# Performance work log

Hardware: AMD Instinct MI355X
Metric: run time of the kernel (lower is better)

Reference implementation:

```python
import jax, jax.numpy as jnp
import numpy as np
from jax import lax

B, T, N, E, H = 8, 12, 716, 10, 64
DIN = 1 + H  # GCN input dim = x(1) concat state(H)
CS = 1       # conv_steps (predict_time)


def setup_inputs() -> dict:
    key = jax.random.key(0)
    ks = jax.random.split(key, 26)
    def rn(i, shape, s=0.1):
        return jax.random.normal(ks[i], shape, jnp.float32) * s
    data = jax.random.normal(ks[0], (B, T, N, 1), jnp.float32)
    tid = jax.random.uniform(ks[1], (B, T, N, 1), jnp.float32)          # time-of-day in [0,1)
    diw = jax.random.randint(ks[2], (B, T, N, 1), 0, 7).astype(jnp.float32)  # day-of-week
    source = jnp.concatenate([data, tid, diw], axis=-1)
    return dict(
        source=source,
        node_embeddings=rn(3, (N, E), 1.0),
        tid_emb=rn(4, (288, E), 1.0),
        diw_emb=rn(5, (7, E), 1.0),
        wp_g=rn(6, (2, E, 2, DIN, 2 * H)),
        bp_g=rn(7, (2, E, 2 * H)),
        fc1W_g=rn(8, (2, 16, DIN)), fc1b_g=rn(9, (2, 16)),
        fc2W_g=rn(10, (2, 2, 16)), fc2b_g=rn(11, (2, 2)),
        fc3W_g=rn(12, (2, E, 2)), fc3b_g=rn(13, (2, E)),
        wp_u=rn(14, (2, E, 2, DIN, H)),
        bp_u=rn(15, (2, E, H)),
        fc1W_u=rn(16, (2, 16, DIN)), fc1b_u=rn(17, (2, 16)),
        fc2W_u=rn(18, (2, 2, 16)), fc2b_u=rn(19, (2, 2)),
        fc3W_u=rn(20, (2, E, 2)), fc3b_u=rn(21, (2, E)),
        predW=rn(22, (2, T, CS, H)),
        predB=rn(23, (2, T)),
        skipW=rn(24, (T, CS, H)),
        skipB=rn(25, (T,)),
    )


def _gcn(x, emb_t, static, wp, bp, fc):
    # x: [B,N,DIN], emb_t: [B,N,E], static: [N,E]
    fc1W, fc1b, fc2W, fc2b, fc3W, fc3b = fc
    h = jax.nn.sigmoid(x @ fc1W.T + fc1b)
    h = jax.nn.sigmoid(h @ fc2W.T + fc2b)
    x_ = h @ fc3W.T + fc3b                            # [B,N,E]
    nodevec = jnp.tanh(emb_t * x_)                    # [B,N,E]
    graph = jax.nn.relu(jnp.einsum('bne,bme->bnm', nodevec, nodevec))
    d = jnp.sum(graph, axis=-1) ** -0.5               # [B,N]
    L = d[:, :, None] * graph * d[:, None, :]         # D^-1/2 A D^-1/2 support
    xg2 = jnp.einsum('bnm,bmc->bnc', L, x)
    w = jnp.einsum('ne,ekio->nkio', static, wp)       # [N,2,DIN,out]
    b = static @ bp                                   # [N,out]
    # support1 is identity -> x_g1 == x
    return (jnp.einsum('bni,nio->bno', x, w[:, 0])
            + jnp.einsum('bni,nio->bno', xg2, w[:, 1]) + b)


def _gru_layer(x_seq, emb_seq, static, gate_p, upd_p):
    # x_seq: [T,B,N,1], emb_seq: [T,B,N,E]
    wp_g, bp_g, fc_g = gate_p
    wp_u, bp_u, fc_u = upd_p
    Hd = wp_u.shape[-1]
    def step(state, inp):
        x, emb = inp
        xs = jnp.concatenate([x, state], axis=-1)
        zr = jax.nn.sigmoid(_gcn(xs, emb, static, wp_g, bp_g, fc_g))
        z, r = jnp.split(zr, 2, axis=-1)
        cand = jnp.concatenate([x, z * state], axis=-1)
        hc = jnp.tanh(_gcn(cand, emb, static, wp_u, bp_u, fc_u))
        h = r * state + (1 - r) * hc
        return h, h
    h0 = jnp.zeros(x_seq.shape[1:3] + (Hd,), x_seq.dtype)
    _, hs = lax.scan(step, h0, (x_seq, emb_seq))
    return hs  # [T,B,N,H]


def reference(source, node_embeddings, tid_emb, diw_emb,
              wp_g, bp_g, fc1W_g, fc1b_g, fc2W_g, fc2b_g, fc3W_g, fc3b_g,
              wp_u, bp_u, fc1W_u, fc1b_u, fc2W_u, fc2b_u, fc3W_u, fc3b_u,
              predW, predB, skipW, skipB):
    x = source[..., :1]                                   # [B,T,N,1]
    tid_idx = (source[..., 1] * 288).astype(jnp.int32)
    diw_idx = source[..., 2].astype(jnp.int32)
    emb = node_embeddings * tid_emb[tid_idx] * diw_emb[diw_idx]  # [B,T,N,E]
    x_t = jnp.moveaxis(x, 1, 0)                           # [T,B,N,1]
    emb_t = jnp.moveaxis(emb, 1, 0)                       # [T,B,N,E]
    cur = x_t
    predict = jnp.zeros((x.shape[0], T, x.shape[2], 1), x.dtype)
    for c in range(2):  # two structurally distinct GRU layers
        gate_p = (wp_g[c], bp_g[c], (fc1W_g[c], fc1b_g[c], fc2W_g[c], fc2b_g[c], fc3W_g[c], fc3b_g[c]))
        upd_p = (wp_u[c], bp_u[c], (fc1W_u[c], fc1b_u[c], fc2W_u[c], fc2b_u[c], fc3W_u[c], fc3b_u[c]))
        hs = _gru_layer(cur, emb_t, node_embeddings, gate_p, upd_p)
        ci = jnp.moveaxis(hs[-CS:], 0, 1)                 # [B,CS,N,H] (dropout is identity in eval)
        out = jnp.einsum('bcnh,och->bon', ci, predW[c]) + predB[c][None, :, None]
        predict = predict + out[..., None]                # [B,T,N,1]
        if c == 0:
            sk = jnp.einsum('bcnh,och->bon', ci, skipW) + skipB[None, :, None]
            cur = x_t - jnp.moveaxis(sk[..., None], 1, 0)
    return predict
```

## Files before the change

### kernel.cpp

```cpp
#include <hip/hip_runtime.h>
#include <math.h>

#define BB 8
#define TT 12
#define NN 716
#define EE 10
#define HH 64
#define DIN 65
#define OG 128
#define OU 64
#define XSP 68
#define JS 32
#define JRX 23
#define NTN 128
#define NP 768
#define NI4 17
#define NVP 12

__device__ __forceinline__ float sigmf(float x){ return 1.0f/(1.0f+__expf(-x)); }

__global__ void k_emb(const float* __restrict__ src, const float* __restrict__ ne,
                      const float* __restrict__ te, const float* __restrict__ de,
                      float* __restrict__ emb, float* __restrict__ cur){
  int idx = blockIdx.x*256 + threadIdx.x;
  if (idx >= BB*TT*NN) return;
  int n = idx % NN; int t = (idx/NN) % TT; int b = idx/(NN*TT);
  const float* s = src + (size_t)idx*3;
  float x = s[0];
  int ti = (int)(s[1]*288.0f);
  int di = (int)(s[2]);
  size_t eo = ((size_t)b*TT + t)*NN*EE + (size_t)n*EE;
  #pragma unroll
  for (int e=0;e<EE;e++)
    emb[eo+e] = ne[n*EE+e]*te[ti*EE+e]*de[di*EE+e];
  cur[((size_t)t*BB + b)*NN + n] = x;
}

__global__ __launch_bounds__(256) void k_prep_w4m(
    const float* __restrict__ ne, const float* __restrict__ wp_g,
    const float* __restrict__ wp_u, float* __restrict__ wg4,
    float* __restrict__ wu4)
{
  __shared__ float wps[EE*4*OG];
  int which = blockIdx.z;
  const float* wp = which ? wp_u : wp_g;
  float* w4 = which ? wu4 : wg4;
  int O = which ? OU : OG;
  int ki4 = blockIdx.x;
  int nq  = blockIdx.y;
  int k = ki4/NI4, i4 = ki4 - k*NI4;
  int tid = threadIdx.x;
  for (int idx=tid; idx<EE*4*O; idx+=256){
    int e = idx/(4*O); int rem = idx - e*4*O; int sub = rem/O; int o = rem - sub*O;
    int i = i4*4 + sub;
    wps[idx] = (i<DIN) ? wp[(((size_t)e*2+k)*DIN+i)*O + o] : 0.f;
  }
  __syncthreads();
  int NG = 256/O;
  int o = tid & (O-1), ng = tid / O;
  int n1 = nq*179, n2 = min(NN, n1+179);
  for (int n = n1+ng; n < n2; n += NG){
    float4 a = {0.f,0.f,0.f,0.f};
    #pragma unroll
    for (int e=0;e<EE;e++){
      float nef = ne[n*EE+e];
      a.x += nef*wps[e*4*O + 0*O + o];
      a.y += nef*wps[e*4*O + 1*O + o];
      a.z += nef*wps[e*4*O + 2*O + o];
      a.w += nef*wps[e*4*O + 3*O + o];
    }
    ((float4*)w4)[((size_t)(n*2+k)*NI4 + i4)*O + o] = a;
  }
}

__global__ void k_misc(const float* __restrict__ ne,
                       const float* __restrict__ bp_g, const float* __restrict__ bp_u,
                       float* __restrict__ bg, float* __restrict__ bu,
                       float* __restrict__ h, const float* __restrict__ cur_c,
                       const float* __restrict__ f1W, const float* __restrict__ f1b,
                       const float* __restrict__ f2W, const float* __restrict__ f2b,
                       const float* __restrict__ f3W, const float* __restrict__ f3b,
                       const float* __restrict__ emb,
                       float* __restrict__ xsg, float* __restrict__ nv){
  int mt = blockIdx.x*256 + threadIdx.x;
  int MT = gridDim.x*256;
  for (int i=mt; i<BB*NN*HH; i+=MT) h[i] = 0.f;
  for (int i=mt; i<NN*OG; i+=MT){
    int o=i&(OG-1), n=i>>7; float a=0.f;
    #pragma unroll
    for (int e=0;e<EE;e++) a += ne[n*EE+e]*bp_g[e*OG+o];
    bg[i]=a;
  }
  for (int i=mt; i<NN*OU; i+=MT){
    int o=i&(OU-1), n=i>>6; float a=0.f;
    #pragma unroll
    for (int e=0;e<EE;e++) a += ne[n*EE+e]*bp_u[e*OU+o];
    bu[i]=a;
  }
  for (int idx=mt; idx<BB*NN; idx+=MT){
    int b=idx/NN, n=idx-b*NN;
    float x = cur_c[(size_t)b*NN + n];
    float* xr = xsg + (size_t)idx*XSP;
    xr[0]=x;
    #pragma unroll
    for (int i2=1;i2<XSP;i2++) xr[i2]=0.f;
    float h1[16];
    #pragma unroll
    for (int k=0;k<16;k++) h1[k]=sigmf(f1b[k]+f1W[k*DIN]*x);
    float h2[2];
    #pragma unroll
    for (int k=0;k<2;k++){
      float s=f2b[k];
      #pragma unroll
      for (int q=0;q<16;q++) s+=f2W[k*16+q]*h1[q];
      h2[k]=sigmf(s);
    }
    #pragma unroll
    for (int e=0;e<EE;e++){
      float xe=f3b[e]+f3W[e*2]*h2[0]+f3W[e*2+1]*h2[1];
      nv[(size_t)idx*EE+e]=tanhf(emb[(((size_t)b*TT+0)*NN+n)*EE+e]*xe);
    }
  }
}

__global__ __launch_bounds__(256) void k_xg2d(
    const float* __restrict__ nv, const float* __restrict__ xs,
    float* __restrict__ parts, float* __restrict__ dout)
{
  __shared__ __align__(16) float nvs[NN*NVP];
  __shared__ __align__(16) float xss[32][XSP];
  __shared__ __align__(16) float gs[32][NTN+4];
  __shared__ float dls[32];
  int js = blockIdx.x, b = blockIdx.y;
  int tid = threadIdx.x;
  int j0 = js*JRX;
  int cnt = NN - j0; if (cnt > JRX) cnt = JRX;
  {
    const float* nvb = nv + (size_t)b*NN*EE;
    for (int idx=tid; idx<NN*EE; idx+=256){
      int n = idx/10, e = idx - n*10;
      nvs[n*NVP+e] = nvb[idx];
    }
  }
  __syncthreads();
  int jg = tid>>5, ns = tid&31;
  float bv[4][EE];
  #pragma unroll
  for (int r=0;r<4;r++){
    int jr = jg*4+r;
    if (jr < cnt){
      const float* bp2 = &nvs[(j0+jr)*NVP];
      float4 b0 = *(const float4*)bp2;
      float4 b1 = *(const float4*)(bp2+4);
      float2 b2 = *(const float2*)(bp2+8);
      bv[r][0]=b0.x; bv[r][1]=b0.y; bv[r][2]=b0.z; bv[r][3]=b0.w;
      bv[r][4]=b1.x; bv[r][5]=b1.y; bv[r][6]=b1.z; bv[r][7]=b1.w;
      bv[r][8]=b2.x; bv[r][9]=b2.y;
    } else {
      #pragma unroll
      for (int e=0;e<EE;e++) bv[r][e]=0.f;
    }
  }
  {
    float sums[4]={0.f,0.f,0.f,0.f};
    for (int n=ns; n<NN; n+=32){
      const float* ap = &nvs[n*NVP];
      float4 a0 = *(const float4*)ap;
      float4 a1 = *(const float4*)(ap+4);
      float2 a2 = *(const float2*)(ap+8);
      float av[10] = {a0.x,a0.y,a0.z,a0.w,a1.x,a1.y,a1.z,a1.w,a2.x,a2.y};
      #pragma unroll
      for (int r=0;r<4;r++){
        float s=0.f;
        #pragma unroll
        for (int e=0;e<EE;e++) s += bv[r][e]*av[e];
        sums[r] += fmaxf(s,0.f);
      }
    }
    #pragma unroll
    for (int r=0;r<4;r++){
      float s = sums[r];
      s += __shfl_xor(s,1,64); s += __shfl_xor(s,2,64);
      s += __shfl_xor(s,4,64); s += __shfl_xor(s,8,64);
      s += __shfl_xor(s,16,64);
      sums[r] = s;
    }
    if (ns==0){
      #pragma unroll
      for (int r=0;r<4;r++){
        int jr = jg*4+r;
        if (jr < cnt){
          float dv = rsqrtf(sums[r]);
          dls[jr] = dv;
          dout[b*NN + j0 + jr] = dv;
        }
      }
    }
  }
  __syncthreads();
  for (int idx=tid; idx<32*XSP; idx+=256){
    int r = idx/XSP, ii = idx - r*XSP;
    float v = 0.f;
    if (r < cnt && ii <= 64)
      v = dls[r]*xs[((size_t)b*NN+j0+r)*XSP + ii];
    xss[r][ii] = v;
  }
  int ng = tid >> 3, ig = tid & 7;
  int ng4 = tid & 31;
  for (int nc=0; nc<6; ++nc){
    int n0 = nc*NTN;
    {
      float g[4][4];
      #pragma unroll
      for (int r=0;r<4;r++){ g[r][0]=0;g[r][1]=0;g[r][2]=0;g[r][3]=0; }
      #pragma unroll
      for (int s2=0;s2<4;s2++){
        int n = n0 + ng4*4 + s2;
        if (n < NN){
          const float* ap = &nvs[n*NVP];
          float4 a0 = *(const float4*)ap;
          float4 a1 = *(const float4*)(ap+4);
          float2 a2 = *(const float2*)(ap+8);
          float av[10] = {a0.x,a0.y,a0.z,a0.w,a1.x,a1.y,a1.z,a1.w,a2.x,a2.y};
          #pragma unroll
          for (int r=0;r<4;r++){
            float s=0.f;
            #pragma unroll
            for (int e=0;e<EE;e++) s += bv[r][e]*av[e];
            g[r][s2] = s;
          }
        }
      }
      #pragma unroll
      for (int r=0;r<4;r++){
        float4 v = { fmaxf(g[r][0],0.f), fmaxf(g[r][1],0.f),
                     fmaxf(g[r][2],0.f), fmaxf(g[r][3],0.f) };
        *(float4*)&gs[jg*4+r][ng4*4] = v;
      }
    }
    __syncthreads();
    {
      float acc[4][8];
      #pragma unroll
      for (int r=0;r<4;r++)
        #pragma unroll
        for (int s2=0;s2<8;s2++) acc[r][s2]=0.f;
      for (int jj=0; jj<cnt; ++jj){
        float4 g4  = *(const float4*)&gs[jj][ng*4];
        float4 x4a = *(const float4*)&xss[jj][ig*8];
        float4 x4b = *(const float4*)&xss[jj][ig*8+4];
        float gr[4] = {g4.x, g4.y, g4.z, g4.w};
        float xr[8] = {x4a.x,x4a.y,x4a.z,x4a.w, x4b.x,x4b.y,x4b.z,x4b.w};
        #pragma unroll
        for (int r=0;r<4;r++)
          #pragma unroll
          for (int s2=0;s2<8;s2++) acc[r][s2] += gr[r]*xr[s2];
      }
      #pragma unroll
      for (int r=0;r<4;r++){
        int n = n0 + ng*4 + r;
        float4 v0 = { acc[r][0], acc[r][1], acc[r][2], acc[r][3] };
        float4 v1 = { acc[r][4], acc[r][5], acc[r][6], acc[r][7] };
        size_t base = (((size_t)js*BB+b)*NP+n)*XSP;
        *(float4*)&parts[base + ig*8]     = v0;
        *(float4*)&parts[base + ig*8 + 4] = v1;
      }
      if (tid < NTN){
        float s = 0.f;
        for (int jj=0; jj<cnt; ++jj) s += gs[jj][tid]*xss[jj][64];
        parts[(((size_t)js*BB+b)*NP + n0+tid)*XSP + 64] = s;
      }
    }
    __syncthreads();
  }
}

__global__ __launch_bounds__(256, 4) void k_tr_gate(
    const float* __restrict__ wg, const float* __restrict__ bg,
    const float* __restrict__ parts, const float* __restrict__ d,
    const float* __restrict__ xsg,
    const float* __restrict__ cur_ct, const float* __restrict__ h,
    const float* __restrict__ emb, int t,
    const float* __restrict__ f1W, const float* __restrict__ f1b,
    const float* __restrict__ f2W, const float* __restrict__ f2b,
    const float* __restrict__ f3W, const float* __restrict__ f3b,
    float* __restrict__ rbuf, float* __restrict__ xsu, float* __restrict__ nv)
{
  __shared__ float xg2s[BB][XSP];
  __shared__ float xss[BB][XSP];
  __shared__ float cs[BB][DIN];
  __shared__ float h1s[BB][16];
  __shared__ float h2s[BB][2];
  int n = blockIdx.x;
  int tid = threadIdx.x;
  for (int idx=tid; idx<BB*XSP; idx+=256){
    int b = idx/XSP, i = idx - b*XSP;
    float s = 0.f;
    if (i < 65){
      #pragma unroll 8
      for (int js2=0; js2<JS; js2++)
        s += parts[(((size_t)js2*BB+b)*NP+n)*XSP + i];
      s *= d[b*NN+n];
    }
    xg2s[b][i] = s;
  }
  for (int idx=tid; idx<BB*XSP; idx+=256){
    int b = idx/XSP, i = idx - b*XSP;
    xss[b][i] = (i<65) ? xsg[((size_t)b*NN+n)*XSP + i] : 0.f;
  }
  __syncthreads();
  {
    int o = tid & 127, half = tid >> 7;
    const float4* w0p = (const float4*)wg + ((size_t)n*2+0)*NI4*OG + o;
    const float4* w1p = w0p + (size_t)NI4*OG;
    float bgv = bg[n*OG+o];
    float acc[4]; acc[0]=bgv; acc[1]=bgv; acc[2]=bgv; acc[3]=bgv;
    #pragma unroll 2
    for (int i4=0;i4<NI4;i4++){
      float4 w0 = w0p[(size_t)i4*OG];
      float4 w1 = w1p[(size_t)i4*OG];
      int i = i4*4;
      #pragma unroll
      for (int bb=0;bb<4;bb++){
        int b = 2*bb+half;
        acc[bb] += xss[b][i]*w0.x + xss[b][i+1]*w0.y
                 + xss[b][i+2]*w0.z + xss[b][i+3]*w0.w
                 + xg2s[b][i]*w1.x + xg2s[b][i+1]*w1.y
                 + xg2s[b][i+2]*w1.z + xg2s[b][i+3]*w1.w;
      }
    }
    #pragma unroll
    for (int bb=0;bb<4;bb++){
      int b = 2*bb+half;
      float v = sigmf(acc[bb]);
      if (o < 64){
        float cv = v * h[((size_t)b*NN+n)*HH + o];
        xsu[((size_t)b*NN+n)*XSP + 1 + o] = cv;
        cs[b][1+o] = cv;
      } else {
        rbuf[((size_t)b*NN+n)*HH + (o-64)] = v;
      }
    }
    if (o == 64){
      #pragma unroll
      for (int bb=0;bb<4;bb++){
        int b = 2*bb+half;
        float x = cur_ct[(size_t)b*NN+n];
        cs[b][0] = x;
        xsu[((size_t)b*NN+n)*XSP] = x;
      }
    }
  }
  __syncthreads();
  if (tid < BB*16){
    int b=tid>>4, k=tid&15;
    const float* wr = f1W + k*DIN;
    float s = f1b[k];
    #pragma unroll
    for (int i=0;i<DIN;i++) s += cs[b][i]*wr[i];
    h1s[b][k] = sigmf(s);
  }
  __syncthreads();
  if (tid < BB*2){
    int b=tid>>1, k=tid&1;
    float s = f2b[k];
    #pragma unroll
    for (int q2=0;q2<16;q2++) s += h1s[b][q2]*f2W[k*16+q2];
    h2s[b][k] = sigmf(s);
  }
  __syncthreads();
  if (tid < BB*EE){
    int b=tid/EE, e=tid-b*EE;
    float xe = f3b[e] + f3W[e*2]*h2s[b][0] + f3W[e*2+1]*h2s[b][1];
    nv[((size_t)b*NN+n)*EE+e] = tanhf(emb[(((size_t)b*TT+t)*NN+n)*EE+e]*xe);
  }
}

__global__ __launch_bounds__(256, 4) void k_tr_upd(
    const float* __restrict__ wu, const float* __restrict__ bu,
    const float* __restrict__ parts, const float* __restrict__ d,
    const float* __restrict__ xsu,
    const float* __restrict__ rbuf, float* __restrict__ h,
    float* __restrict__ cur, int c, int t,
    const float* __restrict__ emb,
    const float* __restrict__ f1W, const float* __restrict__ f1b,
    const float* __restrict__ f2W, const float* __restrict__ f2b,
    const float* __restrict__ f3W, const float* __restrict__ f3b,
    float* __restrict__ xsg, float* __restrict__ nv,
    const float* __restrict__ predW, const float* __restrict__ predB,
    const float* __restrict__ skipW, const float* __restrict__ skipB,
    float* __restrict__ out)
{
  __shared__ float xg2s[BB][XSP];
  __shared__ float xss[BB][XSP];
  __shared__ float hs[BB][HH];
  __shared__ float h1s[BB][16];
  __shared__ float h2s[BB][2];
  __shared__ float xns[BB];
  int n = blockIdx.x;
  int tid = threadIdx.x;
  for (int idx=tid; idx<BB*XSP; idx+=256){
    int b = idx/XSP, i = idx - b*XSP;
    float s = 0.f;
    if (i < 65){
      #pragma unroll 8
      for (int js2=0; js2<JS; js2++)
        s += parts[(((size_t)js2*BB+b)*NP+n)*XSP + i];
      s *= d[b*NN+n];
    }
    xg2s[b][i] = s;
  }
  for (int idx=tid; idx<BB*XSP; idx+=256){
    int b = idx/XSP, i = idx - b*XSP;
    xss[b][i] = (i<65) ? xsu[((size_t)b*NN+n)*XSP + i] : 0.f;
  }
  __syncthreads();
  {
    int o = tid & 63, grp = tid >> 6;
    const float4* w0p = (const float4*)wu + ((size_t)n*2+0)*NI4*OU + o;
    const float4* w1p = w0p + (size_t)NI4*OU;
    float acc[2];
    acc[0] = bu[n*OU+o]; acc[1] = acc[0];
    #pragma unroll 2
    for (int i4=0;i4<NI4;i4++){
      float4 w0 = w0p[(size_t)i4*OU];
      float4 w1 = w1p[(size_t)i4*OU];
      int i = i4*4;
      #pragma unroll
      for (int bb=0;bb<2;bb++){
        int b = grp + 4*bb;
        acc[bb] += xss[b][i]*w0.x + xss[b][i+1]*w0.y
                 + xss[b][i+2]*w0.z + xss[b][i+3]*w0.w
                 + xg2s[b][i]*w1.x + xg2s[b][i+1]*w1.y
                 + xg2s[b][i+2]*w1.z + xg2s[b][i+3]*w1.w;
      }
    }
    #pragma unroll
    for (int bb=0;bb<2;bb++){
      int b = grp + 4*bb;
      float hc = tanhf(acc[bb]);
      float r = rbuf[((size_t)b*NN+n)*HH+o];
      float hold = h[((size_t)b*NN+n)*HH+o];
      float hn = r*hold + (1.f-r)*hc;
      h[((size_t)b*NN+n)*HH+o] = hn;
      hs[b][o] = hn;
    }
  }
  __syncthreads();
  if (t < TT-1){
    if (tid < BB){
      float x = cur[(((size_t)c*TT + (t+1))*BB + tid)*NN + n];
      xns[tid] = x;
      xsg[((size_t)tid*NN+n)*XSP] = x;
    }
    for (int idx=tid; idx<BB*HH; idx+=256){
      int b = idx>>6, oo = idx&63;
      xsg[((size_t)b*NN+n)*XSP + 1 + oo] = hs[b][oo];
    }
    __syncthreads();
    if (tid < BB*16){
      int b=tid>>4, k=tid&15;
      const float* wr = f1W + k*DIN;
      float s = f1b[k] + wr[0]*xns[b];
      #pragma unroll
      for (int oo=0;oo<HH;oo++) s += hs[b][oo]*wr[1+oo];
      h1s[b][k] = sigmf(s);
    }
    __syncthreads();
    if (tid < BB*2){
      int b=tid>>1, k=tid&1;
      float s = f2b[k];
      #pragma unroll
      for (int q2=0;q2<16;q2++) s += h1s[b][q2]*f2W[k*16+q2];
      h2s[b][k] = sigmf(s);
    }
    __syncthreads();
    if (tid < BB*EE){
      int b=tid/EE, e=tid-b*EE;
      float xe = f3b[e] + f3W[e*2]*h2s[b][0] + f3W[e*2+1]*h2s[b][1];
      nv[((size_t)b*NN+n)*EE+e] =
        tanhf(emb[(((size_t)b*TT+(t+1))*NN+n)*EE+e]*xe);
    }
  } else {
    if (tid < BB*TT){
      int b = tid/TT, ot = tid - b*TT;
      const float* pw = predW + ((size_t)c*TT + ot)*HH;
      float pv = predB[c*TT+ot];
      #pragma unroll
      for (int q2=0;q2<HH;q2++) pv += hs[b][q2]*pw[q2];
      size_t oi = ((size_t)b*TT+ot)*NN + n;
      if (c == 0){
        out[oi] = pv;
        const float* sw = skipW + (size_t)ot*HH;
        float sk = skipB[ot];
        #pragma unroll
        for (int q2=0;q2<HH;q2++) sk += hs[b][q2]*sw[q2];
        cur[(((size_t)TT+ot)*BB + b)*NN + n] =
            cur[((size_t)ot*BB + b)*NN + n] - sk;
      } else {
        out[oi] += pv;
      }
    }
  }
}

extern "C" void kernel_launch(void* const* d_in, const int* in_sizes, int n_in,
                              void* d_out, int out_size, void* d_ws, size_t ws_size,
                              hipStream_t stream){
  const float* src  = (const float*)d_in[0];
  const float* ne   = (const float*)d_in[1];
  const float* te   = (const float*)d_in[2];
  const float* de   = (const float*)d_in[3];
  const float* wp_g = (const float*)d_in[4];
  const float* bp_g = (const float*)d_in[5];
  const float* f1W_g= (const float*)d_in[6];
  const float* f1b_g= (const float*)d_in[7];
  const float* f2W_g= (const float*)d_in[8];
  const float* f2b_g= (const float*)d_in[9];
  const float* f3W_g= (const float*)d_in[10];
  const float* f3b_g= (const float*)d_in[11];
  const float* wp_u = (const float*)d_in[12];
  const float* bp_u = (const float*)d_in[13];
  const float* f1W_u= (const float*)d_in[14];
  const float* f1b_u= (const float*)d_in[15];
  const float* f2W_u= (const float*)d_in[16];
  const float* f2b_u= (const float*)d_in[17];
  const float* f3W_u= (const float*)d_in[18];
  const float* f3b_u= (const float*)d_in[19];
  const float* predW= (const float*)d_in[20];
  const float* predB= (const float*)d_in[21];
  const float* skipW= (const float*)d_in[22];
  const float* skipB= (const float*)d_in[23];

  float* ws   = (float*)d_ws;
  float* emb  = ws;
  float* cur  = emb  + (size_t)BB*TT*NN*EE;
  float* wg   = cur  + (size_t)2*TT*BB*NN;
  float* bg   = wg   + (size_t)NN*2*NI4*OG*4;
  float* wu   = bg   + (size_t)NN*OG;
  float* bu   = wu   + (size_t)NN*2*NI4*OU*4;
  float* h    = bu   + (size_t)NN*OU;
  float* xsg  = h    + (size_t)BB*NN*HH;
  float* xsu  = xsg  + (size_t)BB*NN*XSP;
  float* nv   = xsu  + (size_t)BB*NN*XSP;
  float* dbuf = nv   + (size_t)BB*NN*EE;
  float* parts= dbuf + (size_t)BB*NN;
  float* rbuf = parts+ (size_t)JS*BB*NP*XSP;
  float* outp = (float*)d_out;

  k_emb<<<(BB*TT*NN+255)/256, 256, 0, stream>>>(src, ne, te, de, emb, cur);

  for (int c=0;c<2;c++){
    k_prep_w4m<<<dim3(2*NI4,4,2),256,0,stream>>>(ne,
        wp_g + (size_t)c*EE*2*DIN*OG, wp_u + (size_t)c*EE*2*DIN*OU, wg, wu);
    k_misc<<<1024,256,0,stream>>>(ne, bp_g + (size_t)c*EE*OG, bp_u + (size_t)c*EE*OU,
        bg, bu, h, cur + (size_t)c*TT*BB*NN,
        f1W_g + c*16*DIN, f1b_g + c*16, f2W_g + c*32, f2b_g + c*2,
        f3W_g + c*EE*2, f3b_g + c*EE, emb, xsg, nv);
    for (int t=0;t<TT;t++){
      k_xg2d<<<dim3(JS,BB),256,0,stream>>>(nv, xsg, parts, dbuf);
      k_tr_gate<<<NN,256,0,stream>>>(wg, bg, parts, dbuf, xsg,
          cur + ((size_t)c*TT+t)*BB*NN, h, emb, t,
          f1W_u + c*16*DIN, f1b_u + c*16, f2W_u + c*32, f2b_u + c*2,
          f3W_u + c*EE*2, f3b_u + c*EE, rbuf, xsu, nv);
      k_xg2d<<<dim3(JS,BB),256,0,stream>>>(nv, xsu, parts, dbuf);
      k_tr_upd<<<NN,256,0,stream>>>(wu, bu, parts, dbuf, xsu, rbuf, h,
          cur, c, t, emb,
          f1W_g + c*16*DIN, f1b_g + c*16, f2W_g + c*32, f2b_g + c*2,
          f3W_g + c*EE*2, f3b_g + c*EE,
          xsg, nv, predW, predB, skipW, skipB, outp);
    }
  }
}
```

Baseline: 2.968 ms.

## Double k_xg2d threads to 512 and merge prep kernels into one launch

The graph/aggregation kernel now runs with 512 threads per block. Each thread computes one graph row against 8 nodes, accumulates a 4x4 output tile instead of 4x8, and the degree reduction is done across full 64-lane wavefronts. The intent is more parallelism and latency hiding in the per-timestep kernel, which is launched 48 times and only has 256 blocks. Separately, the weight-prep and misc init kernels are fused into one launch using a third grid-z slice, which saves one launch per layer. The cost is fewer FMAs per shared-memory load and more block-level synchronisation pressure.

Result: slower. 3.030 ms (+2.1%).

```diff
diff --git a/kernel.cpp b/kernel.cpp
--- a/kernel.cpp
+++ b/kernel.cpp
@@ -36,94 +36,94 @@
   cur[((size_t)t*BB + b)*NN + n] = x;
 }
 
-__global__ __launch_bounds__(256) void k_prep_w4m(
+__global__ __launch_bounds__(256) void k_prep_all(
     const float* __restrict__ ne, const float* __restrict__ wp_g,
     const float* __restrict__ wp_u, float* __restrict__ wg4,
-    float* __restrict__ wu4)
+    float* __restrict__ wu4,
+    const float* __restrict__ bp_g, const float* __restrict__ bp_u,
+    float* __restrict__ bg, float* __restrict__ bu,
+    float* __restrict__ h, const float* __restrict__ cur_c,
+    const float* __restrict__ f1W, const float* __restrict__ f1b,
+    const float* __restrict__ f2W, const float* __restrict__ f2b,
+    const float* __restrict__ f3W, const float* __restrict__ f3b,
+    const float* __restrict__ emb,
+    float* __restrict__ xsg, float* __restrict__ nv)
 {
   __shared__ float wps[EE*4*OG];
-  int which = blockIdx.z;
-  const float* wp = which ? wp_u : wp_g;
-  float* w4 = which ? wu4 : wg4;
-  int O = which ? OU : OG;
-  int ki4 = blockIdx.x;
-  int nq  = blockIdx.y;
-  int k = ki4/NI4, i4 = ki4 - k*NI4;
+  int z = blockIdx.z;
   int tid = threadIdx.x;
-  for (int idx=tid; idx<EE*4*O; idx+=256){
-    int e = idx/(4*O); int rem = idx - e*4*O; int sub = rem/O; int o = rem - sub*O;
-    int i = i4*4 + sub;
-    wps[idx] = (i<DIN) ? wp[(((size_t)e*2+k)*DIN+i)*O + o] : 0.f;
-  }
-  __syncthreads();
-  int NG = 256/O;
-  int o = tid & (O-1), ng = tid / O;
-  int n1 = nq*179, n2 = min(NN, n1+179);
-  for (int n = n1+ng; n < n2; n += NG){
-    float4 a = {0.f,0.f,0.f,0.f};
-    #pragma unroll
-    for (int e=0;e<EE;e++){
-      float nef = ne[n*EE+e];
-      a.x += nef*wps[e*4*O + 0*O + o];
-      a.y += nef*wps[e*4*O + 1*O + o];
-      a.z += nef*wps[e*4*O + 2*O + o];
-      a.w += nef*wps[e*4*O + 3*O + o];
-    }
-    ((float4*)w4)[((size_t)(n*2+k)*NI4 + i4)*O + o] = a;
+  if (z < 2){
+    const float* wp = z ? wp_u : wp_g;
+    float* w4 = z ? wu4 : wg4;
+    int O = z ? OU : OG;
+    int ki4 = blockIdx.x;
+    int nq  = blockIdx.y;
+    int k = ki4/NI4, i4 = ki4 - k*NI4;
+    for (int idx=tid; idx<EE*4*O; idx+=256){
+      int e = idx/(4*O); int rem = idx - e*4*O; int sub = rem/O; int o = rem - sub*O;
+      int i = i4*4 + sub;
+      wps[idx] = (i<DIN) ? wp[(((size_t)e*2+k)*DIN+i)*O + o] : 0.f;
+    }
+    __syncthreads();
+    int NG = 256/O;
+    int o = tid & (O-1), ng = tid / O;
+    int n1 = nq*179, n2 = min(NN, n1+179);
+    for (int n = n1+ng; n < n2; n += NG){
+      float4 a = {0.f,0.f,0.f,0.f};
+      #pragma unroll
+      for (int e=0;e<EE;e++){
+        float nef = ne[n*EE+e];
+        a.x += nef*wps[e*4*O + 0*O + o];
+        a.y += nef*wps[e*4*O + 1*O + o];
+        a.z += nef*wps[e*4*O + 2*O + o];
+        a.w += nef*wps[e*4*O + 3*O + o];
+      }
+      ((float4*)w4)[((size_t)(n*2+k)*NI4 + i4)*O + o] = a;
+    }
+  } else {
+    int mt = (blockIdx.x*4 + blockIdx.y)*256 + tid;
+    const int MT = 136*256;
+    for (int i=mt; i<BB*NN*HH; i+=MT) h[i] = 0.f;
+    for (int i=mt; i<NN*OG; i+=MT){
+      int o=i&(OG-1), n=i>>7; float a=0.f;
+      #pragma unroll
+      for (int e=0;e<EE;e++) a += ne[n*EE+e]*bp_g[e*OG+o];
+      bg[i]=a;
+    }
+    for (int i=mt; i<NN*OU; i+=MT){
+      int o=i&(OU-1), n=i>>6; float a=0.f;
+      #pragma unroll
+      for (int e=0;e<EE;e++) a += ne[n*EE+e]*bp_u[e*OU+o];
+      bu[i]=a;
+    }
+    for (int idx=mt; idx<BB*NN; idx+=MT){
+      int b=idx/NN, n=idx-b*NN;
+      float x = cur_c[(size_t)b*NN + n];
+      float* xr = xsg + (size_t)idx*XSP;
+      xr[0]=x;
+      #pragma unroll
+      for (int i2=1;i2<XSP;i2++) xr[i2]=0.f;
+      float h1[16];
+      #pragma unroll
+      for (int k=0;k<16;k++) h1[k]=sigmf(f1b[k]+f1W[k*DIN]*x);
+      float h2[2];
+      #pragma unroll
+      for (int k=0;k<2;k++){
+        float s=f2b[k];
+        #pragma unroll
+        for (int q=0;q<16;q++) s+=f2W[k*16+q]*h1[q];
+        h2[k]=sigmf(s);
+      }
+      #pragma unroll
+      for (int e=0;e<EE;e++){
+        float xe=f3b[e]+f3W[e*2]*h2[0]+f3W[e*2+1]*h2[1];
+        nv[(size_t)idx*EE+e]=tanhf(emb[(((size_t)b*TT+0)*NN+n)*EE+e]*xe);
+      }
+    }
   }
 }
 
-__global__ void k_misc(const float* __restrict__ ne,
-                       const float* __restrict__ bp_g, const float* __restrict__ bp_u,
-                       float* __restrict__ bg, float* __restrict__ bu,
-                       float* __restrict__ h, const float* __restrict__ cur_c,
-                       const float* __restrict__ f1W, const float* __restrict__ f1b,
-                       const float* __restrict__ f2W, const float* __restrict__ f2b,
-                       const float* __restrict__ f3W, const float* __restrict__ f3b,
-                       const float* __restrict__ emb,
-                       float* __restrict__ xsg, float* __restrict__ nv){
-  int mt = blockIdx.x*256 + threadIdx.x;
-  int MT = gridDim.x*256;
-  for (int i=mt; i<BB*NN*HH; i+=MT) h[i] = 0.f;
-  for (int i=mt; i<NN*OG; i+=MT){
-    int o=i&(OG-1), n=i>>7; float a=0.f;
-    #pragma unroll
-    for (int e=0;e<EE;e++) a += ne[n*EE+e]*bp_g[e*OG+o];
-    bg[i]=a;
-  }
-  for (int i=mt; i<NN*OU; i+=MT){
-    int o=i&(OU-1), n=i>>6; float a=0.f;
-    #pragma unroll
-    for (int e=0;e<EE;e++) a += ne[n*EE+e]*bp_u[e*OU+o];
-    bu[i]=a;
-  }
-  for (int idx=mt; idx<BB*NN; idx+=MT){
-    int b=idx/NN, n=idx-b*NN;
-    float x = cur_c[(size_t)b*NN + n];
-    float* xr = xsg + (size_t)idx*XSP;
-    xr[0]=x;
-    #pragma unroll
-    for (int i2=1;i2<XSP;i2++) xr[i2]=0.f;
-    float h1[16];
-    #pragma unroll
-    for (int k=0;k<16;k++) h1[k]=sigmf(f1b[k]+f1W[k*DIN]*x);
-    float h2[2];
-    #pragma unroll
-    for (int k=0;k<2;k++){
-      float s=f2b[k];
-      #pragma unroll
-      for (int q=0;q<16;q++) s+=f2W[k*16+q]*h1[q];
-      h2[k]=sigmf(s);
-    }
-    #pragma unroll
-    for (int e=0;e<EE;e++){
-      float xe=f3b[e]+f3W[e*2]*h2[0]+f3W[e*2+1]*h2[1];
-      nv[(size_t)idx*EE+e]=tanhf(emb[(((size_t)b*TT+0)*NN+n)*EE+e]*xe);
-    }
-  }
-}
-
-__global__ __launch_bounds__(256) void k_xg2d(
+__global__ __launch_bounds__(512) void k_xg2d(
     const float* __restrict__ nv, const float* __restrict__ xs,
     float* __restrict__ parts, float* __restrict__ dout)
 {
@@ -137,58 +137,58 @@
   int cnt = NN - j0; if (cnt > JRX) cnt = JRX;
   {
     const float* nvb = nv + (size_t)b*NN*EE;
-    for (int idx=tid; idx<NN*EE; idx+=256){
+    for (int idx=tid; idx<NN*EE; idx+=512){
       int n = idx/10, e = idx - n*10;
       nvs[n*NVP+e] = nvb[idx];
     }
   }
   __syncthreads();
-  int jg = tid>>5, ns = tid&31;
-  float bv[4][EE];
-  #pragma unroll
-  for (int r=0;r<4;r++){
-    int jr = jg*4+r;
-    if (jr < cnt){
-      const float* bp2 = &nvs[(j0+jr)*NVP];
-      float4 b0 = *(const float4*)bp2;
-      float4 b1 = *(const float4*)(bp2+4);
-      float2 b2 = *(const float2*)(bp2+8);
-      bv[r][0]=b0.x; bv[r][1]=b0.y; bv[r][2]=b0.z; bv[r][3]=b0.w;
-      bv[r][4]=b1.x; bv[r][5]=b1.y; bv[r][6]=b1.z; bv[r][7]=b1.w;
-      bv[r][8]=b2.x; bv[r][9]=b2.y;
-    } else {
-      #pragma unroll
-      for (int e=0;e<EE;e++) bv[r][e]=0.f;
-    }
-  }
   {
-    float sums[4]={0.f,0.f,0.f,0.f};
-    for (int n=ns; n<NN; n+=32){
+    int wv = tid>>6, lane = tid&63;
+    float bvd[3][EE];
+    #pragma unroll
+    for (int r=0;r<3;r++){
+      int jr = wv*3+r;
+      if (jr < cnt){
+        const float* bp2 = &nvs[(j0+jr)*NVP];
+        float4 b0 = *(const float4*)bp2;
+        float4 b1 = *(const float4*)(bp2+4);
+        float2 b2 = *(const float2*)(bp2+8);
+        bvd[r][0]=b0.x; bvd[r][1]=b0.y; bvd[r][2]=b0.z; bvd[r][3]=b0.w;
+        bvd[r][4]=b1.x; bvd[r][5]=b1.y; bvd[r][6]=b1.z; bvd[r][7]=b1.w;
+        bvd[r][8]=b2.x; bvd[r][9]=b2.y;
+      } else {
+        #pragma unroll
+        for (int e=0;e<EE;e++) bvd[r][e]=0.f;
+      }
+    }
+    float sums[3]={0.f,0.f,0.f};
+    for (int n=lane; n<NN; n+=64){
       const float* ap = &nvs[n*NVP];
       float4 a0 = *(const float4*)ap;
       float4 a1 = *(const float4*)(ap+4);
       float2 a2 = *(const float2*)(ap+8);
       float av[10] = {a0.x,a0.y,a0.z,a0.w,a1.x,a1.y,a1.z,a1.w,a2.x,a2.y};
       #pragma unroll
-      for (int r=0;r<4;r++){
+      for (int r=0;r<3;r++){
         float s=0.f;
         #pragma unroll
-        for (int e=0;e<EE;e++) s += bv[r][e]*av[e];
+        for (int e=0;e<EE;e++) s += bvd[r][e]*av[e];
         sums[r] += fmaxf(s,0.f);
       }
     }
     #pragma unroll
-    for (int r=0;r<4;r++){
+    for (int r=0;r<3;r++){
       float s = sums[r];
       s += __shfl_xor(s,1,64); s += __shfl_xor(s,2,64);
       s += __shfl_xor(s,4,64); s += __shfl_xor(s,8,64);
-      s += __shfl_xor(s,16,64);
+      s += __shfl_xor(s,16,64); s += __shfl_xor(s,32,64);
       sums[r] = s;
     }
-    if (ns==0){
-      #pragma unroll
-      for (int r=0;r<4;r++){
-        int jr = jg*4+r;
+    if (lane==0){
+      #pragma unroll
+      for (int r=0;r<3;r++){
+        int jr = wv*3+r;
         if (jr < cnt){
           float dv = rsqrtf(sums[r]);
           dls[jr] = dv;
@@ -198,72 +198,73 @@
     }
   }
   __syncthreads();
-  for (int idx=tid; idx<32*XSP; idx+=256){
+  for (int idx=tid; idx<32*XSP; idx+=512){
     int r = idx/XSP, ii = idx - r*XSP;
     float v = 0.f;
     if (r < cnt && ii <= 64)
       v = dls[r]*xs[((size_t)b*NN+j0+r)*XSP + ii];
     xss[r][ii] = v;
   }
-  int ng = tid >> 3, ig = tid & 7;
-  int ng4 = tid & 31;
+  int jrow = tid >> 4;
+  int ng3  = tid & 15;
+  float bvg[EE];
+  if (jrow < cnt){
+    const float* bp2 = &nvs[(j0+jrow)*NVP];
+    float4 b0 = *(const float4*)bp2;
+    float4 b1 = *(const float4*)(bp2+4);
+    float2 b2 = *(const float2*)(bp2+8);
+    bvg[0]=b0.x; bvg[1]=b0.y; bvg[2]=b0.z; bvg[3]=b0.w;
+    bvg[4]=b1.x; bvg[5]=b1.y; bvg[6]=b1.z; bvg[7]=b1.w;
+    bvg[8]=b2.x; bvg[9]=b2.y;
+  } else {
+    #pragma unroll
+    for (int e=0;e<EE;e++) bvg[e]=0.f;
+  }
+  int ngg = tid >> 4;
+  int ig  = tid & 15;
   for (int nc=0; nc<6; ++nc){
     int n0 = nc*NTN;
     {
-      float g[4][4];
-      #pragma unroll
-      for (int r=0;r<4;r++){ g[r][0]=0;g[r][1]=0;g[r][2]=0;g[r][3]=0; }
-      #pragma unroll
-      for (int s2=0;s2<4;s2++){
-        int n = n0 + ng4*4 + s2;
+      float g[8];
+      #pragma unroll
+      for (int s2=0;s2<8;s2++){
+        int n = n0 + ng3*8 + s2;
+        float s = 0.f;
         if (n < NN){
           const float* ap = &nvs[n*NVP];
           float4 a0 = *(const float4*)ap;
           float4 a1 = *(const float4*)(ap+4);
           float2 a2 = *(const float2*)(ap+8);
-          float av[10] = {a0.x,a0.y,a0.z,a0.w,a1.x,a1.y,a1.z,a1.w,a2.x,a2.y};
-          #pragma unroll
-          for (int r=0;r<4;r++){
-            float s=0.f;
-            #pragma unroll
-            for (int e=0;e<EE;e++) s += bv[r][e]*av[e];
-            g[r][s2] = s;
-          }
+          s = bvg[0]*a0.x + bvg[1]*a0.y + bvg[2]*a0.z + bvg[3]*a0.w
+            + bvg[4]*a1.x + bvg[5]*a1.y + bvg[6]*a1.z + bvg[7]*a1.w
+            + bvg[8]*a2.x + bvg[9]*a2.y;
         }
-      }
-      #pragma unroll
-      for (int r=0;r<4;r++){
-        float4 v = { fmaxf(g[r][0],0.f), fmaxf(g[r][1],0.f),
-                     fmaxf(g[r][2],0.f), fmaxf(g[r][3],0.f) };
-        *(float4*)&gs[jg*4+r][ng4*4] = v;
-      }
+        g[s2] = fmaxf(s, 0.f);
+      }
+      float4 v0 = { g[0],g[1],g[2],g[3] };
+      float4 v1 = { g[4],g[5],g[6],g[7] };
+      *(float4*)&gs[jrow][ng3*8]   = v0;
+      *(float4*)&gs[jrow][ng3*8+4] = v1;
     }
     __syncthreads();
     {
-      float acc[4][8];
-      #pragma unroll
-      for (int r=0;r<4;r++)
-        #pragma unroll
-        for (int s2=0;s2<8;s2++) acc[r][s2]=0.f;
+      float acc[4][4];
+      #pragma unroll
+      for (int r=0;r<4;r++){ acc[r][0]=0;acc[r][1]=0;acc[r][2]=0;acc[r][3]=0; }
       for (int jj=0; jj<cnt; ++jj){
-        float4 g4  = *(const float4*)&gs[jj][ng*4];
-        float4 x4a = *(const float4*)&xss[jj][ig*8];
-        float4 x4b = *(const float4*)&xss[jj][ig*8+4];
+        float4 g4 = *(const float4*)&gs[jj][ngg*4];
+        float4 x4 = *(const float4*)&xss[jj][ig*4];
         float gr[4] = {g4.x, g4.y, g4.z, g4.w};
-        float xr[8] = {x4a.x,x4a.y,x4a.z,x4a.w, x4b.x,x4b.y,x4b.z,x4b.w};
-        #pragma unroll
-        for (int r=0;r<4;r++)
-          #pragma unroll
-          for (int s2=0;s2<8;s2++) acc[r][s2] += gr[r]*xr[s2];
+        acc[0][0]+=gr[0]*x4.x; acc[0][1]+=gr[0]*x4.y; acc[0][2]+=gr[0]*x4.z; acc[0][3]+=gr[0]*x4.w;
+        acc[1][0]+=gr[1]*x4.x; acc[1][1]+=gr[1]*x4.y; acc[1][2]+=gr[1]*x4.z; acc[1][3]+=gr[1]*x4.w;
+        acc[2][0]+=gr[2]*x4.x; acc[2][1]+=gr[2]*x4.y; acc[2][2]+=gr[2]*x4.z; acc[2][3]+=gr[2]*x4.w;
+        acc[3][0]+=gr[3]*x4.x; acc[3][1]+=gr[3]*x4.y; acc[3][2]+=gr[3]*x4.z; acc[3][3]+=gr[3]*x4.w;
       }
       #pragma unroll
       for (int r=0;r<4;r++){
-        int n = n0 + ng*4 + r;
-        float4 v0 = { acc[r][0], acc[r][1], acc[r][2], acc[r][3] };
-        float4 v1 = { acc[r][4], acc[r][5], acc[r][6], acc[r][7] };
-        size_t base = (((size_t)js*BB+b)*NP+n)*XSP;
-        *(float4*)&parts[base + ig*8]     = v0;
-        *(float4*)&parts[base + ig*8 + 4] = v1;
+        int n = n0 + ngg*4 + r;
+        float4 v = { acc[r][0], acc[r][1], acc[r][2], acc[r][3] };
+        *(float4*)&parts[(((size_t)js*BB+b)*NP+n)*XSP + ig*4] = v;
       }
       if (tid < NTN){
         float s = 0.f;
@@ -551,19 +552,19 @@
   k_emb<<<(BB*TT*NN+255)/256, 256, 0, stream>>>(src, ne, te, de, emb, cur);
 
   for (int c=0;c<2;c++){
-    k_prep_w4m<<<dim3(2*NI4,4,2),256,0,stream>>>(ne,
-        wp_g + (size_t)c*EE*2*DIN*OG, wp_u + (size_t)c*EE*2*DIN*OU, wg, wu);
-    k_misc<<<1024,256,0,stream>>>(ne, bp_g + (size_t)c*EE*OG, bp_u + (size_t)c*EE*OU,
-        bg, bu, h, cur + (size_t)c*TT*BB*NN,
+    k_prep_all<<<dim3(2*NI4,4,3),256,0,stream>>>(ne,
+        wp_g + (size_t)c*EE*2*DIN*OG, wp_u + (size_t)c*EE*2*DIN*OU, wg, wu,
+        bp_g + (size_t)c*EE*OG, bp_u + (size_t)c*EE*OU, bg, bu,
+        h, cur + (size_t)c*TT*BB*NN,
         f1W_g + c*16*DIN, f1b_g + c*16, f2W_g + c*32, f2b_g + c*2,
         f3W_g + c*EE*2, f3b_g + c*EE, emb, xsg, nv);
     for (int t=0;t<TT;t++){
-      k_xg2d<<<dim3(JS,BB),256,0,stream>>>(nv, xsg, parts, dbuf);
+      k_xg2d<<<dim3(JS,BB),512,0,stream>>>(nv, xsg, parts, dbuf);
       k_tr_gate<<<NN,256,0,stream>>>(wg, bg, parts, dbuf, xsg,
           cur + ((size_t)c*TT+t)*BB*NN, h, emb, t,
           f1W_u + c*16*DIN, f1b_u + c*16, f2W_u + c*32, f2b_u + c*2,
           f3W_u + c*EE*2, f3b_u + c*EE, rbuf, xsu, nv);
-      k_xg2d<<<dim3(JS,BB),256,0,stream>>>(nv, xsu, parts, dbuf);
+      k_xg2d<<<dim3(JS,BB),512,0,stream>>>(nv, xsu, parts, dbuf);
       k_tr_upd<<<NN,256,0,stream>>>(wu, bu, parts, dbuf, xsu, rbuf, h,
           cur, c, t, emb,
           f1W_g + c*16*DIN, f1b_g + c*16, f2W_g + c*32, f2b_g + c*2,
```

## Transpose node-vector smem layout, fold degree scaling into graph tile, merge prep kernels

Applied to the files above, without the earlier changes.

Stores the node vectors in shared memory transposed ([E][768], zero-padded) so lanes read consecutive n without strided float4 loads. The D^-1/2 row scaling is moved from the staged x rows into the relu'd graph tile, which lets the x staging loop run before the first barrier. The two per-layer prep kernels are merged into one launch using an extra grid z-slice, removing a launch. The misc work now runs on only 136 blocks instead of 1024, which may lengthen that phase.

New measurement: 2.899 ms. 1.02x faster.

```diff
diff --git a/kernel.cpp b/kernel.cpp
--- a/kernel.cpp
+++ b/kernel.cpp
@@ -15,7 +15,7 @@
 #define NTN 128
 #define NP 768
 #define NI4 17
-#define NVP 12
+#define NVT 768
 
 __device__ __forceinline__ float sigmf(float x){ return 1.0f/(1.0f+__expf(-x)); }
 
@@ -36,89 +36,89 @@
   cur[((size_t)t*BB + b)*NN + n] = x;
 }
 
-__global__ __launch_bounds__(256) void k_prep_w4m(
+__global__ __launch_bounds__(256) void k_prep_all(
     const float* __restrict__ ne, const float* __restrict__ wp_g,
     const float* __restrict__ wp_u, float* __restrict__ wg4,
-    float* __restrict__ wu4)
+    float* __restrict__ wu4,
+    const float* __restrict__ bp_g, const float* __restrict__ bp_u,
+    float* __restrict__ bg, float* __restrict__ bu,
+    float* __restrict__ h, const float* __restrict__ cur_c,
+    const float* __restrict__ f1W, const float* __restrict__ f1b,
+    const float* __restrict__ f2W, const float* __restrict__ f2b,
+    const float* __restrict__ f3W, const float* __restrict__ f3b,
+    const float* __restrict__ emb,
+    float* __restrict__ xsg, float* __restrict__ nv)
 {
   __shared__ float wps[EE*4*OG];
-  int which = blockIdx.z;
-  const float* wp = which ? wp_u : wp_g;
-  float* w4 = which ? wu4 : wg4;
-  int O = which ? OU : OG;
-  int ki4 = blockIdx.x;
-  int nq  = blockIdx.y;
-  int k = ki4/NI4, i4 = ki4 - k*NI4;
+  int z = blockIdx.z;
   int tid = threadIdx.x;
-  for (int idx=tid; idx<EE*4*O; idx+=256){
-    int e = idx/(4*O); int rem = idx - e*4*O; int sub = rem/O; int o = rem - sub*O;
-    int i = i4*4 + sub;
-    wps[idx] = (i<DIN) ? wp[(((size_t)e*2+k)*DIN+i)*O + o] : 0.f;
-  }
-  __syncthreads();
-  int NG = 256/O;
-  int o = tid & (O-1), ng = tid / O;
-  int n1 = nq*179, n2 = min(NN, n1+179);
-  for (int n = n1+ng; n < n2; n += NG){
-    float4 a = {0.f,0.f,0.f,0.f};
-    #pragma unroll
-    for (int e=0;e<EE;e++){
-      float nef = ne[n*EE+e];
-      a.x += nef*wps[e*4*O + 0*O + o];
-      a.y += nef*wps[e*4*O + 1*O + o];
-      a.z += nef*wps[e*4*O + 2*O + o];
-      a.w += nef*wps[e*4*O + 3*O + o];
-    }
-    ((float4*)w4)[((size_t)(n*2+k)*NI4 + i4)*O + o] = a;
-  }
-}
-
-__global__ void k_misc(const float* __restrict__ ne,
-                       const float* __restrict__ bp_g, const float* __restrict__ bp_u,
-                       float* __restrict__ bg, float* __restrict__ bu,
-                       float* __restrict__ h, const float* __restrict__ cur_c,
-                       const float* __restrict__ f1W, const float* __restrict__ f1b,
-                       const float* __restrict__ f2W, const float* __restrict__ f2b,
-                       const float* __restrict__ f3W, const float* __restrict__ f3b,
-                       const float* __restrict__ emb,
-                       float* __restrict__ xsg, float* __restrict__ nv){
-  int mt = blockIdx.x*256 + threadIdx.x;
-  int MT = gridDim.x*256;
-  for (int i=mt; i<BB*NN*HH; i+=MT) h[i] = 0.f;
-  for (int i=mt; i<NN*OG; i+=MT){
-    int o=i&(OG-1), n=i>>7; float a=0.f;
-    #pragma unroll
-    for (int e=0;e<EE;e++) a += ne[n*EE+e]*bp_g[e*OG+o];
-    bg[i]=a;
-  }
-  for (int i=mt; i<NN*OU; i+=MT){
-    int o=i&(OU-1), n=i>>6; float a=0.f;
-    #pragma unroll
-    for (int e=0;e<EE;e++) a += ne[n*EE+e]*bp_u[e*OU+o];
-    bu[i]=a;
-  }
-  for (int idx=mt; idx<BB*NN; idx+=MT){
-    int b=idx/NN, n=idx-b*NN;
-    float x = cur_c[(size_t)b*NN + n];
-    float* xr = xsg + (size_t)idx*XSP;
-    xr[0]=x;
-    #pragma unroll
-    for (int i2=1;i2<XSP;i2++) xr[i2]=0.f;
-    float h1[16];
-    #pragma unroll
-    for (int k=0;k<16;k++) h1[k]=sigmf(f1b[k]+f1W[k*DIN]*x);
-    float h2[2];
-    #pragma unroll
-    for (int k=0;k<2;k++){
-      float s=f2b[k];
-      #pragma unroll
-      for (int q=0;q<16;q++) s+=f2W[k*16+q]*h1[q];
-      h2[k]=sigmf(s);
-    }
-    #pragma unroll
-    for (int e=0;e<EE;e++){
-      float xe=f3b[e]+f3W[e*2]*h2[0]+f3W[e*2+1]*h2[1];
-      nv[(size_t)idx*EE+e]=tanhf(emb[(((size_t)b*TT+0)*NN+n)*EE+e]*xe);
+  if (z < 2){
+    const float* wp = z ? wp_u : wp_g;
+    float* w4 = z ? wu4 : wg4;
+    int O = z ? OU : OG;
+    int ki4 = blockIdx.x;
+    int nq  = blockIdx.y;
+    int k = ki4/NI4, i4 = ki4 - k*NI4;
+    for (int idx=tid; idx<EE*4*O; idx+=256){
+      int e = idx/(4*O); int rem = idx - e*4*O; int sub = rem/O; int o = rem - sub*O;
+      int i = i4*4 + sub;
+      wps[idx] = (i<DIN) ? wp[(((size_t)e*2+k)*DIN+i)*O + o] : 0.f;
+    }
+    __syncthreads();
+    int NG = 256/O;
+    int o = tid & (O-1), ng = tid / O;
+    int n1 = nq*179, n2 = min(NN, n1+179);
+    for (int n = n1+ng; n < n2; n += NG){
+      float4 a = {0.f,0.f,0.f,0.f};
+      #pragma unroll
+      for (int e=0;e<EE;e++){
+        float nef = ne[n*EE+e];
+        a.x += nef*wps[e*4*O + 0*O + o];
+        a.y += nef*wps[e*4*O + 1*O + o];
+        a.z += nef*wps[e*4*O + 2*O + o];
+        a.w += nef*wps[e*4*O + 3*O + o];
+      }
+      ((float4*)w4)[((size_t)(n*2+k)*NI4 + i4)*O + o] = a;
+    }
+  } else {
+    int mt = (blockIdx.x*4 + blockIdx.y)*256 + tid;
+    const int MT = 136*256;
+    for (int i=mt; i<BB*NN*HH; i+=MT) h[i] = 0.f;
+    for (int i=mt; i<NN*OG; i+=MT){
+      int o=i&(OG-1), n=i>>7; float a=0.f;
+      #pragma unroll
+      for (int e=0;e<EE;e++) a += ne[n*EE+e]*bp_g[e*OG+o];
+      bg[i]=a;
+    }
+    for (int i=mt; i<NN*OU; i+=MT){
+      int o=i&(OU-1), n=i>>6; float a=0.f;
+      #pragma unroll
+      for (int e=0;e<EE;e++) a += ne[n*EE+e]*bp_u[e*OU+o];
+      bu[i]=a;
+    }
+    for (int idx=mt; idx<BB*NN; idx+=MT){
+      int b=idx/NN, n=idx-b*NN;
+      float x = cur_c[(size_t)b*NN + n];
+      float* xr = xsg + (size_t)idx*XSP;
+      xr[0]=x;
+      #pragma unroll
+      for (int i2=1;i2<XSP;i2++) xr[i2]=0.f;
+      float h1[16];
+      #pragma unroll
+      for (int k=0;k<16;k++) h1[k]=sigmf(f1b[k]+f1W[k*DIN]*x);
+      float h2[2];
+      #pragma unroll
+      for (int k=0;k<2;k++){
+        float s=f2b[k];
+        #pragma unroll
+        for (int q=0;q<16;q++) s+=f2W[k*16+q]*h1[q];
+        h2[k]=sigmf(s);
+      }
+      #pragma unroll
+      for (int e=0;e<EE;e++){
+        float xe=f3b[e]+f3W[e*2]*h2[0]+f3W[e*2+1]*h2[1];
+        nv[(size_t)idx*EE+e]=tanhf(emb[(((size_t)b*TT+0)*NN+n)*EE+e]*xe);
+      }
     }
   }
 }
@@ -127,7 +127,7 @@
     const float* __restrict__ nv, const float* __restrict__ xs,
     float* __restrict__ parts, float* __restrict__ dout)
 {
-  __shared__ __align__(16) float nvs[NN*NVP];
+  __shared__ __align__(16) float nvsT[EE][NVT];
   __shared__ __align__(16) float xss[32][XSP];
   __shared__ __align__(16) float gs[32][NTN+4];
   __shared__ float dls[32];
@@ -138,8 +138,19 @@
   {
     const float* nvb = nv + (size_t)b*NN*EE;
     for (int idx=tid; idx<NN*EE; idx+=256){
-      int n = idx/10, e = idx - n*10;
-      nvs[n*NVP+e] = nvb[idx];
+      int n = idx/EE, e = idx - n*EE;
+      nvsT[e][n] = nvb[idx];
+    }
+    for (int idx=tid; idx<EE*(NVT-NN); idx+=256){
+      int e = idx/(NVT-NN), n = NN + (idx - e*(NVT-NN));
+      nvsT[e][n] = 0.f;
+    }
+    for (int idx=tid; idx<32*XSP; idx+=256){
+      int r = idx/XSP, ii = idx - r*XSP;
+      float v = 0.f;
+      if (r < cnt && ii <= 64)
+        v = xs[((size_t)b*NN+j0+r)*XSP + ii];
+      xss[r][ii] = v;
     }
   }
   __syncthreads();
@@ -148,27 +159,16 @@
   #pragma unroll
   for (int r=0;r<4;r++){
     int jr = jg*4+r;
-    if (jr < cnt){
-      const float* bp2 = &nvs[(j0+jr)*NVP];
-      float4 b0 = *(const float4*)bp2;
-      float4 b1 = *(const float4*)(bp2+4);
-      float2 b2 = *(const float2*)(bp2+8);
-      bv[r][0]=b0.x; bv[r][1]=b0.y; bv[r][2]=b0.z; bv[r][3]=b0.w;
-      bv[r][4]=b1.x; bv[r][5]=b1.y; bv[r][6]=b1.z; bv[r][7]=b1.w;
-      bv[r][8]=b2.x; bv[r][9]=b2.y;
-    } else {
-      #pragma unroll
-      for (int e=0;e<EE;e++) bv[r][e]=0.f;
-    }
+    bool ok = (jr < cnt);
+    #pragma unroll
+    for (int e=0;e<EE;e++) bv[r][e] = ok ? nvsT[e][j0+jr] : 0.f;
   }
   {
     float sums[4]={0.f,0.f,0.f,0.f};
     for (int n=ns; n<NN; n+=32){
-      const float* ap = &nvs[n*NVP];
-      float4 a0 = *(const float4*)ap;
-      float4 a1 = *(const float4*)(ap+4);
-      float2 a2 = *(const float2*)(ap+8);
-      float av[10] = {a0.x,a0.y,a0.z,a0.w,a1.x,a1.y,a1.z,a1.w,a2.x,a2.y};
+      float av[EE];
+      #pragma unroll
+      for (int e=0;e<EE;e++) av[e] = nvsT[e][n];
       #pragma unroll
       for (int r=0;r<4;r++){
         float s=0.f;
@@ -198,44 +198,24 @@
     }
   }
   __syncthreads();
-  for (int idx=tid; idx<32*XSP; idx+=256){
-    int r = idx/XSP, ii = idx - r*XSP;
-    float v = 0.f;
-    if (r < cnt && ii <= 64)
-      v = dls[r]*xs[((size_t)b*NN+j0+r)*XSP + ii];
-    xss[r][ii] = v;
-  }
+  float dl[4];
+  #pragma unroll
+  for (int r=0;r<4;r++){ int jr=jg*4+r; dl[r] = (jr<cnt)? dls[jr] : 0.f; }
   int ng = tid >> 3, ig = tid & 7;
-  int ng4 = tid & 31;
   for (int nc=0; nc<6; ++nc){
     int n0 = nc*NTN;
-    {
-      float g[4][4];
-      #pragma unroll
-      for (int r=0;r<4;r++){ g[r][0]=0;g[r][1]=0;g[r][2]=0;g[r][3]=0; }
-      #pragma unroll
-      for (int s2=0;s2<4;s2++){
-        int n = n0 + ng4*4 + s2;
-        if (n < NN){
-          const float* ap = &nvs[n*NVP];
-          float4 a0 = *(const float4*)ap;
-          float4 a1 = *(const float4*)(ap+4);
-          float2 a2 = *(const float2*)(ap+8);
-          float av[10] = {a0.x,a0.y,a0.z,a0.w,a1.x,a1.y,a1.z,a1.w,a2.x,a2.y};
-          #pragma unroll
-          for (int r=0;r<4;r++){
-            float s=0.f;
-            #pragma unroll
-            for (int e=0;e<EE;e++) s += bv[r][e]*av[e];
-            g[r][s2] = s;
-          }
-        }
-      }
+    #pragma unroll
+    for (int k=0;k<4;k++){
+      int n = n0 + ns + 32*k;
+      float av[EE];
+      #pragma unroll
+      for (int e=0;e<EE;e++) av[e] = nvsT[e][n];
       #pragma unroll
       for (int r=0;r<4;r++){
-        float4 v = { fmaxf(g[r][0],0.f), fmaxf(g[r][1],0.f),
-                     fmaxf(g[r][2],0.f), fmaxf(g[r][3],0.f) };
-        *(float4*)&gs[jg*4+r][ng4*4] = v;
+        float s=0.f;
+        #pragma unroll
+        for (int e=0;e<EE;e++) s += bv[r][e]*av[e];
+        gs[jg*4+r][ns + 32*k] = fmaxf(s,0.f)*dl[r];
       }
     }
     __syncthreads();
@@ -551,10 +531,10 @@
   k_emb<<<(BB*TT*NN+255)/256, 256, 0, stream>>>(src, ne, te, de, emb, cur);
 
   for (int c=0;c<2;c++){
-    k_prep_w4m<<<dim3(2*NI4,4,2),256,0,stream>>>(ne,
-        wp_g + (size_t)c*EE*2*DIN*OG, wp_u + (size_t)c*EE*2*DIN*OU, wg, wu);
-    k_misc<<<1024,256,0,stream>>>(ne, bp_g + (size_t)c*EE*OG, bp_u + (size_t)c*EE*OU,
-        bg, bu, h, cur + (size_t)c*TT*BB*NN,
+    k_prep_all<<<dim3(2*NI4,4,3),256,0,stream>>>(ne,
+        wp_g + (size_t)c*EE*2*DIN*OG, wp_u + (size_t)c*EE*2*DIN*OU, wg, wu,
+        bp_g + (size_t)c*EE*OG, bp_u + (size_t)c*EE*OU, bg, bu,
+        h, cur + (size_t)c*TT*BB*NN,
         f1W_g + c*16*DIN, f1b_g + c*16, f2W_g + c*32, f2b_g + c*2,
         f3W_g + c*EE*2, f3b_g + c*EE, emb, xsg, nv);
     for (int t=0;t<TT;t++){
```
